# Optimization experiments

Hardware: AMD Instinct MI355X
Metric: run time of the kernel (lower is better)

## Reference

```python
import jax, jax.numpy as jnp
import numpy as np

A = 4096          # agents
N_OBJ = 8192      # objects
IN_DIM = 16       # input_dim
EMBED = 128       # embedding_dim
MAX_OBJ = 16      # max set size
DEG = 8           # communicate in-degree (constant, target-major edges)
OBS_DEG = 8       # observe degree
POS_DIM = 2
ORIG = IN_DIM + POS_DIM   # 18, decoded element dim
THRES = 0.02              # duplicate filter distance threshold


def setup_inputs() -> dict:
    key = jax.random.key(0)
    ks = jax.random.split(key, 16)
    def lin(k, fi, fo):
        return (jax.random.normal(k, (fi, fo), jnp.float32) / np.float32(np.sqrt(fi)))
    obj_x = jax.random.normal(ks[0], (N_OBJ, IN_DIM), jnp.float32)
    obj_pos = jax.random.uniform(ks[1], (N_OBJ, POS_DIM), jnp.float32) * 10.0
    agent_pos = jax.random.uniform(ks[2], (A, POS_DIM), jnp.float32) * 10.0
    # (agent, observe, object) edges: row0 = agent, row1 = object (as in the torch HeteroData)
    obs_tgt = jnp.repeat(jnp.arange(A), OBS_DEG)
    obs_src = jax.random.randint(ks[3], (A * OBS_DEG,), 0, N_OBJ)
    obs_edge_index = jnp.stack([obs_tgt, obs_src])
    # (agent, communicate, agent) edges: row0 = source j, row1 = target i; target-major, constant degree
    tgt = jnp.repeat(jnp.arange(A), DEG)
    src = (tgt + 1 + jnp.tile(jnp.arange(DEG), A)) % A
    comm_edge_index = jnp.stack([src, tgt])
    return dict(
        obj_x=obj_x, obj_pos=obj_pos, agent_pos=agent_pos,
        enc_W1=lin(ks[4], ORIG, EMBED), enc_b1=jnp.zeros((EMBED,), jnp.float32),
        enc_W2=lin(ks[5], EMBED, EMBED), enc_b2=jnp.zeros((EMBED,), jnp.float32),
        mdec_Ws=lin(ks[6], EMBED, MAX_OBJ + 1), mdec_bs=jnp.zeros((MAX_OBJ + 1,), jnp.float32),
        mdec_Wx=lin(ks[7], EMBED, MAX_OBJ * ORIG), mdec_bx=jnp.zeros((MAX_OBJ * ORIG,), jnp.float32),
        menc_W1=lin(ks[8], ORIG, EMBED), menc_b1=jnp.zeros((EMBED,), jnp.float32),
        menc_W2=lin(ks[9], EMBED, EMBED), menc_b2=jnp.zeros((EMBED,), jnp.float32),
        dec_Ws=lin(ks[10], EMBED, MAX_OBJ + 1), dec_bs=jnp.zeros((MAX_OBJ + 1,), jnp.float32),
        dec_Wx=lin(ks[11], EMBED, MAX_OBJ * ORIG), dec_bx=jnp.zeros((MAX_OBJ * ORIG,), jnp.float32),
        obs_edge_index=obs_edge_index, comm_edge_index=comm_edge_index,
    )


def reference(obj_x, obj_pos, agent_pos,
              enc_W1, enc_b1, enc_W2, enc_b2,
              mdec_Ws, mdec_bs, mdec_Wx, mdec_bx,
              menc_W1, menc_b1, menc_W2, menc_b2,
              dec_Ws, dec_bs, dec_Wx, dec_bx,
              obs_edge_index, comm_edge_index):
    nA = agent_pos.shape[0]
    # ---- EncodeGNN: edge_index.flip -> source = object (row1), target = agent (row0)
    o = obs_edge_index[1]
    a = obs_edge_index[0]
    # message: [x_j, posx_j - posa_i] (position='rel')
    msg = jnp.concatenate([obj_x[o], obj_pos[o] - agent_pos[a]], axis=-1)      # [E_obs, ORIG]
    h = jax.nn.relu(msg @ enc_W1 + enc_b1)
    enc = jax.ops.segment_sum(h, a, num_segments=nA) @ enc_W2 + enc_b2         # [A, EMBED]
    # ---- MergeGNN message: decode source embedding per communicate edge
    j = comm_edge_index[0]
    i = comm_edge_index[1]
    zj = enc[j]                                                                 # [E, EMBED]
    npred = jnp.argmax(zj @ mdec_Ws + mdec_bs, axis=-1)                         # predicted set size per edge
    elems = (zj @ mdec_Wx + mdec_bx).reshape(-1, MAX_OBJ, ORIG)                 # [E, MAX_OBJ, ORIG]
    # update_rel_pos: decoded_pos += pos_j - pos_i
    relpos = (agent_pos[j] - agent_pos[i])[:, None, :]
    elems = jnp.concatenate([elems[..., :-POS_DIM], elems[..., -POS_DIM:] + relpos], axis=-1)
    valid = jnp.arange(MAX_OBJ)[None, :] < npred[:, None]                       # [E, MAX_OBJ]
    # ---- aggregate: edges are target-major with constant degree -> per-agent candidate pool
    deg = comm_edge_index.shape[1] // nA
    K = deg * MAX_OBJ
    cand = elems.reshape(nA, K, ORIG)
    v = valid.reshape(nA, K)
    # filter_duplicates (pos_only=True): pairwise distance on last POS_DIM dims
    pos = cand[..., -POS_DIM:]
    D = jnp.linalg.norm(pos[:, :, None, :] - pos[:, None, :, :], axis=-1)       # [A, K, K]
    tri = jnp.triu(jnp.ones((K, K), bool), k=1)
    dup = (D < THRES) & tri[None] & v[:, :, None] & v[:, None, :]
    keep = v & ~jnp.any(dup, axis=1)                                            # column is dup of an earlier row
    cnt = jnp.cumsum(keep.astype(jnp.int32), axis=1)
    keep = keep & (cnt <= MAX_OBJ - 1)                                          # cap at max_n - 1 kept elements
    # merge_encoder: masked set encode per agent
    hm = jax.nn.relu(cand @ menc_W1 + menc_b1) * keep[..., None]
    merged = hm.sum(axis=1) @ menc_W2 + menc_b2                                 # [A, EMBED]
    # ---- final decoder
    n2 = jnp.argmax(merged @ dec_Ws + dec_bs, axis=-1)
    decoded = (merged @ dec_Wx + dec_bx).reshape(nA, MAX_OBJ, ORIG)
    mask = jnp.arange(MAX_OBJ)[None, :] < n2[:, None]
    decoded = decoded * mask[..., None]                                         # padded+masked ragged set
    batch = jnp.broadcast_to(jnp.arange(nA)[:, None], (nA, MAX_OBJ))
    return decoded, batch, mask
```

## Files before the change

kernel.cpp:

```cpp
#include <hip/hip_runtime.h>

#define A_N   4096
#define EMBED 128
#define MAXO  16
#define DEG   8
#define OBSD  8
#define ORIG  18
#define KCAND 128
#define G     4
#define NBLK  (A_N / G)
#define NTHR  512
#define EL    (MAXO * ORIG)
#define NQ    (MAXO + 1)
#define THRES2 (0.02f * 0.02f)

#define EP_END    288
#define LG_BEG    320
#define LG_END    456

__global__ __launch_bounds__(NTHR, 8) void enc512_kernel(
    const float* __restrict__ obj_x, const float* __restrict__ obj_pos,
    const float* __restrict__ agent_pos,
    const float* __restrict__ enc_W1, const float* __restrict__ enc_b1,
    const float* __restrict__ enc_W2, const float* __restrict__ enc_b2,
    const float* __restrict__ mdec_Ws, const float* __restrict__ mdec_bs,
    const float* __restrict__ mdec_Wx, const float* __restrict__ mdec_bx,
    const int* __restrict__ obs_edge,
    float* __restrict__ elems_base, int* __restrict__ npred_out,
    float2* __restrict__ pxy_base)
{
    const int blk = blockIdx.x, tid = threadIdx.x;
    const int i0  = blk * G;
    const int col = tid & 127, q = tid >> 7;

    __shared__ int    on[G][OBSD];
    __shared__ float  msg[G * OBSD][20];
    __shared__ float4 SG[EMBED];
    __shared__ float4 Ep4[4][EMBED];
    __shared__ float4 Eg[EMBED];
    __shared__ float  Lp[2][G * NQ];
    __shared__ float  lgts[G][NQ];
    __shared__ float4 Pp[2][EL];

    if (tid < G * OBSD) {
        const int g = tid >> 3, d = tid & 7;
        on[g][d] = obs_edge[A_N * OBSD + (i0 + g) * OBSD + d];
    }
    __syncthreads();
    for (int idx = tid; idx < G * OBSD * ORIG; idx += NTHR) {
        const int r = idx / ORIG, c = idx % ORIG;
        const int g = r >> 3, d = r & 7;
        const int o = on[g][d];
        float v;
        if (c < 16) v = obj_x[o * 16 + c];
        else        v = obj_pos[o * 2 + (c - 16)] - agent_pos[(i0 + g) * 2 + (c - 16)];
        msg[r][c] = v;
    }
    __syncthreads();

    {
        float w1[ORIG];
#pragma unroll
        for (int c = 0; c < ORIG; ++c) w1[c] = enc_W1[c * EMBED + col];
        const float b1 = enc_b1[col];
        float acc = 0.f;
#pragma unroll
        for (int d = 0; d < OBSD; ++d) {
            const int r = q * OBSD + d;
            const float4* mr = (const float4*)&msg[r][0];
            const float4 m0 = mr[0], m1 = mr[1], m2 = mr[2], m3 = mr[3];
            const float2 m4 = *(const float2*)&msg[r][16];
            float h = b1
                + m0.x*w1[0]  + m0.y*w1[1]  + m0.z*w1[2]  + m0.w*w1[3]
                + m1.x*w1[4]  + m1.y*w1[5]  + m1.z*w1[6]  + m1.w*w1[7]
                + m2.x*w1[8]  + m2.y*w1[9]  + m2.z*w1[10] + m2.w*w1[11]
                + m3.x*w1[12] + m3.y*w1[13] + m3.z*w1[14] + m3.w*w1[15]
                + m4.x*w1[16] + m4.y*w1[17];
            acc += fmaxf(h, 0.f);
        }
        ((float*)&SG[col])[q] = acc;
    }
    __syncthreads();

    {
        float4 acc = {0.f, 0.f, 0.f, 0.f};
        const int c0 = 32 * q;
#pragma unroll 8
        for (int c = c0; c < c0 + 32; ++c) {
            const float4 s = SG[c];
            const float  w = enc_W2[c * EMBED + col];
            acc.x += s.x * w; acc.y += s.y * w; acc.z += s.z * w; acc.w += s.w * w;
        }
        Ep4[q][col] = acc;
    }
    __syncthreads();
    if (tid < EMBED) {
        const float4 a = Ep4[0][tid], b = Ep4[1][tid], c = Ep4[2][tid], d = Ep4[3][tid];
        const float bb = enc_b2[tid];
        float4 e;
        e.x = a.x + b.x + c.x + d.x + bb;
        e.y = a.y + b.y + c.y + d.y + bb;
        e.z = a.z + b.z + c.z + d.z + bb;
        e.w = a.w + b.w + c.w + d.w + bb;
        Eg[tid] = e;
    }
    __syncthreads();

    if (tid < EP_END) {
        const int pp = tid / 144, pe = tid % 144;
        const int e0 = 2 * pe;
        float4 a0 = {0.f,0.f,0.f,0.f}, a1 = {0.f,0.f,0.f,0.f};
        const int c0 = 64 * pp;
#pragma unroll 8
        for (int c = c0; c < c0 + 64; ++c) {
            const float4 s = Eg[c];
            const float2 w2 = *(const float2*)&mdec_Wx[c * EL + e0];
            a0.x += s.x*w2.x; a0.y += s.y*w2.x; a0.z += s.z*w2.x; a0.w += s.w*w2.x;
            a1.x += s.x*w2.y; a1.y += s.y*w2.y; a1.z += s.z*w2.y; a1.w += s.w*w2.y;
        }
        Pp[pp][e0] = a0; Pp[pp][e0 + 1] = a1;
    } else if (tid >= LG_BEG && tid < LG_END) {
        const int lu = tid - LG_BEG, pp = lu / 68, lq = lu % 68;
        const int g = lq / NQ, qq = lq % NQ;
        float v = 0.f;
        const int c0 = 64 * pp;
#pragma unroll 8
        for (int c = c0; c < c0 + 64; ++c)
            v += ((const float*)&Eg[c])[g] * mdec_Ws[c * NQ + qq];
        Lp[pp][lq] = v;
    }
    __syncthreads();

    if (tid < EL) {
        const float4 a = Pp[0][tid], b = Pp[1][tid];
        const float bx = mdec_bx[tid];
        elems_base[(size_t)(i0 + 0) * EL + tid] = a.x + b.x + bx;
        elems_base[(size_t)(i0 + 1) * EL + tid] = a.y + b.y + bx;
        elems_base[(size_t)(i0 + 2) * EL + tid] = a.z + b.z + bx;
        elems_base[(size_t)(i0 + 3) * EL + tid] = a.w + b.w + bx;
    } else if (tid < EL + G * NQ) {
        const int lq = tid - EL;
        const int g = lq / NQ, qq = lq % NQ;
        lgts[g][qq] = Lp[0][lq] + Lp[1][lq] + mdec_bs[qq];
    } else if (tid < EL + G * NQ + G * MAXO) {
        const int u = tid - (EL + G * NQ);
        const int g = u >> 4, m = u & 15;
        const int e16 = m * ORIG + 16, e17 = e16 + 1;
        const float px = ((const float*)&Pp[0][e16])[g] + ((const float*)&Pp[1][e16])[g]
                       + mdec_bx[e16];
        const float py = ((const float*)&Pp[0][e17])[g] + ((const float*)&Pp[1][e17])[g]
                       + mdec_bx[e17];
        pxy_base[(size_t)(i0 + g) * MAXO + m] = make_float2(px, py);
    }
    __syncthreads();
    if (tid < G) {
        int best = 0; float bv = lgts[tid][0];
        for (int qq = 1; qq < NQ; ++qq) if (lgts[tid][qq] > bv) { bv = lgts[tid][qq]; best = qq; }
        npred_out[i0 + tid] = best;
    }
}

__global__ __launch_bounds__(NTHR, 8) void merge512_kernel(
    const float* __restrict__ agent_pos,
    const float* __restrict__ menc_W1, const float* __restrict__ menc_b1,
    const float* __restrict__ menc_W2, const float* __restrict__ menc_b2,
    const float* __restrict__ dec_Ws, const float* __restrict__ dec_bs,
    const float* __restrict__ dec_Wx, const float* __restrict__ dec_bx,
    const int* __restrict__ comm_edge,
    const float* __restrict__ elems_base, const int* __restrict__ npred,
    const float2* __restrict__ pxy_base,
    float* __restrict__ out_dec, float* __restrict__ out_batch,
    float* __restrict__ out_mask)
{
    const int blk = blockIdx.x, tid = threadIdx.x;
    const int i0  = blk * G;
    const int col = tid & 127, q = tid >> 7;
    const int lane = tid & 63, wv = tid >> 6;
    const int w = wv >> 1, half = wv & 1;

    __shared__ int    jn[G][DEG];
    __shared__ float  relx[G][DEG], rely[G][DEG];
    __shared__ int    npd[G][DEG];
    __shared__ float2 pxy[G][KCAND];
    __shared__ int    vl[G][KCAND];
    __shared__ float2 pv[G][KCAND];
    __shared__ int    wcv[G][2], kcv[G][2];
    __shared__ int    nv[G], kcnt[G];
    __shared__ int    klist[G][MAXO];
    __shared__ float  kc[G][MAXO][20];
    __shared__ float4 Hs[EMBED];
    __shared__ float4 Mp4[4][EMBED];
    __shared__ float4 Mg[EMBED];
    __shared__ float  Lp[2][G * NQ];
    __shared__ float  lg2[G][NQ];
    __shared__ int    n2s[G];
    __shared__ float4 Pp[2][EL];

    if (tid < G * DEG) {
        const int g = tid >> 3, d = tid & 7;
        const int e = (i0 + g) * DEG + d;
        const int j  = comm_edge[e];
        const int ii = comm_edge[A_N * DEG + e];
        jn[g][d]  = j;
        relx[g][d] = agent_pos[j * 2 + 0] - agent_pos[ii * 2 + 0];
        rely[g][d] = agent_pos[j * 2 + 1] - agent_pos[ii * 2 + 1];
        npd[g][d] = npred[j];
    }
    __syncthreads();

    const int k = 64 * half + lane;
    const int kd = k >> 4, km = k & 15;
    float2 p;
    int val;
    {
        p = pxy_base[(size_t)jn[w][kd] * MAXO + km];
        p.x += relx[w][kd]; p.y += rely[w][kd];
        pxy[w][k] = p;
        val = (km < npd[w][kd]) ? 1 : 0;
        const unsigned long long bal = __ballot(val);
        const int pref = (int)__popcll(bal << (63 - lane));
        if (lane == 63) wcv[w][half] = (int)__popcll(bal);
        __syncthreads();
        const int base = half ? wcv[w][0] : 0;
        if (val) { vl[w][base + pref - 1] = k; pv[w][base + pref - 1] = p; }
        if (lane == 0 && half == 0) nv[w] = wcv[w][0] + wcv[w][1];
        __syncthreads();
    }

    {
        const int nvg = nv[w];
        int dup = 0;
        for (int idx = 0; idx < nvg; ++idx) {
            const int k1 = vl[w][idx];
            if (k1 >= k) break;
            const float2 p1 = pv[w][idx];
            const float dx = p1.x - p.x, dy = p1.y - p.y;
            if (dx * dx + dy * dy < THRES2) dup = 1;
        }
        const int kp = (val && !dup) ? 1 : 0;
        const unsigned long long bal = __ballot(kp);
        const int pref = (int)__popcll(bal << (63 - lane));
        if (lane == 63) kcv[w][half] = (int)__popcll(bal);
        __syncthreads();
        const int cnt = (half ? kcv[w][0] : 0) + pref;
        if (kp && cnt <= MAXO - 1) klist[w][cnt - 1] = k;
        if (lane == 0 && half == 0) {
            const int tot = kcv[w][0] + kcv[w][1];
            kcnt[w] = (tot < MAXO - 1) ? tot : (MAXO - 1);
        }
        __syncthreads();
    }

    for (int idx = tid; idx < G * EL; idx += NTHR) {
        const int g = idx / EL, rem = idx % EL;
        const int s = rem / ORIG, c = rem % ORIG;
        if (s < kcnt[g]) {
            const int kk = klist[g][s], d = kk >> 4, m = kk & 15;
            float v;
            if (c < 16) v = elems_base[(size_t)jn[g][d] * EL + m * ORIG + c];
            else        v = (c == 16) ? pxy[g][kk].x : pxy[g][kk].y;
            kc[g][s][c] = v;
        }
    }
    __syncthreads();

    {
        float w1[ORIG];
#pragma unroll
        for (int c = 0; c < ORIG; ++c) w1[c] = menc_W1[c * EMBED + col];
        const float b1 = menc_b1[col];
        const int nk = kcnt[q];
        float hs = 0.f;
        for (int s = 0; s < nk; ++s) {
            const float4* mr = (const float4*)&kc[q][s][0];
            const float4 m0 = mr[0], m1 = mr[1], m2 = mr[2], m3 = mr[3];
            const float2 m4 = *(const float2*)&kc[q][s][16];
            float h = b1
                + m0.x*w1[0]  + m0.y*w1[1]  + m0.z*w1[2]  + m0.w*w1[3]
                + m1.x*w1[4]  + m1.y*w1[5]  + m1.z*w1[6]  + m1.w*w1[7]
                + m2.x*w1[8]  + m2.y*w1[9]  + m2.z*w1[10] + m2.w*w1[11]
                + m3.x*w1[12] + m3.y*w1[13] + m3.z*w1[14] + m3.w*w1[15]
                + m4.x*w1[16] + m4.y*w1[17];
            hs += fmaxf(h, 0.f);
        }
        ((float*)&Hs[col])[q] = hs;
    }
    __syncthreads();

    {
        float4 acc = {0.f, 0.f, 0.f, 0.f};
        const int c0 = 32 * q;
#pragma unroll 8
        for (int c = c0; c < c0 + 32; ++c) {
            const float4 s = Hs[c];
            const float  ww = menc_W2[c * EMBED + col];
            acc.x += s.x * ww; acc.y += s.y * ww; acc.z += s.z * ww; acc.w += s.w * ww;
        }
        Mp4[q][col] = acc;
    }
    __syncthreads();
    if (tid < EMBED) {
        const float4 a = Mp4[0][tid], b = Mp4[1][tid], c = Mp4[2][tid], d = Mp4[3][tid];
        const float bb = menc_b2[tid];
        float4 e;
        e.x = a.x + b.x + c.x + d.x + bb;
        e.y = a.y + b.y + c.y + d.y + bb;
        e.z = a.z + b.z + c.z + d.z + bb;
        e.w = a.w + b.w + c.w + d.w + bb;
        Mg[tid] = e;
    }
    __syncthreads();

    if (tid < EP_END) {
        const int pp = tid / 144, pe = tid % 144;
        const int e0 = 2 * pe;
        float4 a0 = {0.f,0.f,0.f,0.f}, a1 = {0.f,0.f,0.f,0.f};
        const int c0 = 64 * pp;
#pragma unroll 8
        for (int c = c0; c < c0 + 64; ++c) {
            const float4 s = Mg[c];
            const float2 w2 = *(const float2*)&dec_Wx[c * EL + e0];
            a0.x += s.x*w2.x; a0.y += s.y*w2.x; a0.z += s.z*w2.x; a0.w += s.w*w2.x;
            a1.x += s.x*w2.y; a1.y += s.y*w2.y; a1.z += s.z*w2.y; a1.w += s.w*w2.y;
        }
        Pp[pp][e0] = a0; Pp[pp][e0 + 1] = a1;
    } else if (tid >= LG_BEG && tid < LG_END) {
        const int lu = tid - LG_BEG, pp = lu / 68, lq = lu % 68;
        const int g = lq / NQ, qq = lq % NQ;
        float v = 0.f;
        const int c0 = 64 * pp;
#pragma unroll 8
        for (int c = c0; c < c0 + 64; ++c)
            v += ((const float*)&Mg[c])[g] * dec_Ws[c * NQ + qq];
        Lp[pp][lq] = v;
    }
    __syncthreads();

    float4 dreg = {0.f, 0.f, 0.f, 0.f};
    if (tid < EL) {
        const float4 a = Pp[0][tid], b = Pp[1][tid];
        const float bx = dec_bx[tid];
        dreg.x = a.x + b.x + bx; dreg.y = a.y + b.y + bx;
        dreg.z = a.z + b.z + bx; dreg.w = a.w + b.w + bx;
    } else if (tid < EL + G * NQ) {
        const int lq = tid - EL;
        const int g = lq / NQ, qq = lq % NQ;
        lg2[g][qq] = Lp[0][lq] + Lp[1][lq] + dec_bs[qq];
    }
    __syncthreads();
    if (tid < G) {
        int best = 0; float bv = lg2[tid][0];
        for (int qq = 1; qq < NQ; ++qq) if (lg2[tid][qq] > bv) { bv = lg2[tid][qq]; best = qq; }
        n2s[tid] = best;
    }
    __syncthreads();

    if (tid < EL) {
        const int m = tid / ORIG;
        out_dec[(size_t)(i0 + 0) * EL + tid] = (m < n2s[0]) ? dreg.x : 0.f;
        out_dec[(size_t)(i0 + 1) * EL + tid] = (m < n2s[1]) ? dreg.y : 0.f;
        out_dec[(size_t)(i0 + 2) * EL + tid] = (m < n2s[2]) ? dreg.z : 0.f;
        out_dec[(size_t)(i0 + 3) * EL + tid] = (m < n2s[3]) ? dreg.w : 0.f;
    } else if (tid >= NTHR - G * MAXO) {
        const int idx = tid - (NTHR - G * MAXO);
        const int g = idx >> 4, m = idx & 15;
        out_batch[(i0 + g) * MAXO + m] = (float)(i0 + g);
        out_mask[(i0 + g) * MAXO + m]  = (m < n2s[g]) ? 1.f : 0.f;
    }
}

extern "C" void kernel_launch(void* const* d_in, const int* in_sizes, int n_in,
                              void* d_out, int out_size, void* d_ws, size_t ws_size,
                              hipStream_t stream)
{
    const float* obj_x     = (const float*)d_in[0];
    const float* obj_pos   = (const float*)d_in[1];
    const float* agent_pos = (const float*)d_in[2];
    const float* enc_W1    = (const float*)d_in[3];
    const float* enc_b1    = (const float*)d_in[4];
    const float* enc_W2    = (const float*)d_in[5];
    const float* enc_b2    = (const float*)d_in[6];
    const float* mdec_Ws   = (const float*)d_in[7];
    const float* mdec_bs   = (const float*)d_in[8];
    const float* mdec_Wx   = (const float*)d_in[9];
    const float* mdec_bx   = (const float*)d_in[10];
    const float* menc_W1   = (const float*)d_in[11];
    const float* menc_b1   = (const float*)d_in[12];
    const float* menc_W2   = (const float*)d_in[13];
    const float* menc_b2   = (const float*)d_in[14];
    const float* dec_Ws    = (const float*)d_in[15];
    const float* dec_bs    = (const float*)d_in[16];
    const float* dec_Wx    = (const float*)d_in[17];
    const float* dec_bx    = (const float*)d_in[18];
    const int*   obs_edge  = (const int*)d_in[19];
    const int*   comm_edge = (const int*)d_in[20];

    char* ws = (char*)d_ws;
    float*  elems_base = (float*)ws;
    int*    npred      = (int*)(ws + (size_t)A_N * EL * sizeof(float));
    float2* pxy_base   = (float2*)(ws + (size_t)A_N * EL * sizeof(float)
                                      + (size_t)A_N * sizeof(int));

    float* out_dec   = (float*)d_out;
    float* out_batch = out_dec + (size_t)A_N * EL;
    float* out_mask  = out_batch + (size_t)A_N * MAXO;

    enc512_kernel<<<NBLK, NTHR, 0, stream>>>(
        obj_x, obj_pos, agent_pos, enc_W1, enc_b1, enc_W2, enc_b2,
        mdec_Ws, mdec_bs, mdec_Wx, mdec_bx, obs_edge,
        elems_base, npred, pxy_base);

    merge512_kernel<<<NBLK, NTHR, 0, stream>>>(
        agent_pos, menc_W1, menc_b1, menc_W2, menc_b2,
        dec_Ws, dec_bs, dec_Wx, dec_bx, comm_edge,
        elems_base, npred, pxy_base, out_dec, out_batch, out_mask);
}
```

Measured before the change: 153.8 us.

## Pre-fold W2 into decoder weights and unroll duplicate-check scan by two

A new prep kernel multiplies enc_W2/menc_W2 (with their biases) into the downstream decoder weight matrices, so each block no longer runs the 128x128 second-layer matmul or its reduction barriers. The main kernels then apply the folded 128x288 and 128x17 weights directly to the summed hidden layer. The duplicate-filter scan in the merge kernel now reads two candidates per step with vector loads, using sentinel padding at the end of the list. This adds a small extra launch and changes floating-point summation order.

Result: slower. 157.6 us (+2.5%).

```diff
diff --git a/kernel.cpp b/kernel.cpp
--- a/kernel.cpp
+++ b/kernel.cpp
@@ -18,13 +18,55 @@
 #define LG_BEG    320
 #define LG_END    456
 
+__global__ __launch_bounds__(320) void prep_kernel(
+    const float* __restrict__ enc_W2, const float* __restrict__ enc_b2,
+    const float* __restrict__ mdec_Wx, const float* __restrict__ mdec_Ws,
+    const float* __restrict__ mdec_bx, const float* __restrict__ mdec_bs,
+    const float* __restrict__ menc_W2, const float* __restrict__ menc_b2,
+    const float* __restrict__ dec_Wx, const float* __restrict__ dec_Ws,
+    const float* __restrict__ dec_bx, const float* __restrict__ dec_bs,
+    float* __restrict__ fWxA, float* __restrict__ fbxA,
+    float* __restrict__ fWsA, float* __restrict__ fbsA,
+    float* __restrict__ fWxB, float* __restrict__ fbxB,
+    float* __restrict__ fWsB, float* __restrict__ fbsB)
+{
+    const int b = blockIdx.x, tid = threadIdx.x;
+    const int side = b / 129, r = b % 129;
+    const float* W2 = side ? menc_W2 : enc_W2;
+    const float* b2 = side ? menc_b2 : enc_b2;
+    const float* Wx = side ? dec_Wx : mdec_Wx;
+    const float* Ws = side ? dec_Ws : mdec_Ws;
+    const float* bx = side ? dec_bx : mdec_bx;
+    const float* bs = side ? dec_bs : mdec_bs;
+    float* oWx = side ? fWxB : fWxA;
+    float* obx = side ? fbxB : fbxA;
+    float* oWs = side ? fWsB : fWsA;
+    float* obs_ = side ? fbsB : fbsA;
+
+    __shared__ float rv[EMBED];
+    if (tid < EMBED) rv[tid] = (r < EMBED) ? W2[r * EMBED + tid] : b2[tid];
+    __syncthreads();
+
+    if (tid < EL) {
+        float acc = 0.f;
+        for (int t = 0; t < EMBED; ++t) acc += rv[t] * Wx[t * EL + tid];
+        if (r < EMBED) oWx[r * EL + tid] = acc;
+        else           obx[tid] = acc + bx[tid];
+    } else if (tid < EL + NQ) {
+        const int q = tid - EL;
+        float acc = 0.f;
+        for (int t = 0; t < EMBED; ++t) acc += rv[t] * Ws[t * NQ + q];
+        if (r < EMBED) oWs[r * NQ + q] = acc;
+        else           obs_[q] = acc + bs[q];
+    }
+}
+
 __global__ __launch_bounds__(NTHR, 8) void enc512_kernel(
     const float* __restrict__ obj_x, const float* __restrict__ obj_pos,
     const float* __restrict__ agent_pos,
     const float* __restrict__ enc_W1, const float* __restrict__ enc_b1,
-    const float* __restrict__ enc_W2, const float* __restrict__ enc_b2,
-    const float* __restrict__ mdec_Ws, const float* __restrict__ mdec_bs,
-    const float* __restrict__ mdec_Wx, const float* __restrict__ mdec_bx,
+    const float* __restrict__ fWxA, const float* __restrict__ fbxA,
+    const float* __restrict__ fWsA, const float* __restrict__ fbsA,
     const int* __restrict__ obs_edge,
     float* __restrict__ elems_base, int* __restrict__ npred_out,
     float2* __restrict__ pxy_base)
@@ -36,8 +78,6 @@
     __shared__ int    on[G][OBSD];
     __shared__ float  msg[G * OBSD][20];
     __shared__ float4 SG[EMBED];
-    __shared__ float4 Ep4[4][EMBED];
-    __shared__ float4 Eg[EMBED];
     __shared__ float  Lp[2][G * NQ];
     __shared__ float  lgts[G][NQ];
     __shared__ float4 Pp[2][EL];
@@ -82,30 +122,6 @@
     }
     __syncthreads();
 
-    {
-        float4 acc = {0.f, 0.f, 0.f, 0.f};
-        const int c0 = 32 * q;
-#pragma unroll 8
-        for (int c = c0; c < c0 + 32; ++c) {
-            const float4 s = SG[c];
-            const float  w = enc_W2[c * EMBED + col];
-            acc.x += s.x * w; acc.y += s.y * w; acc.z += s.z * w; acc.w += s.w * w;
-        }
-        Ep4[q][col] = acc;
-    }
-    __syncthreads();
-    if (tid < EMBED) {
-        const float4 a = Ep4[0][tid], b = Ep4[1][tid], c = Ep4[2][tid], d = Ep4[3][tid];
-        const float bb = enc_b2[tid];
-        float4 e;
-        e.x = a.x + b.x + c.x + d.x + bb;
-        e.y = a.y + b.y + c.y + d.y + bb;
-        e.z = a.z + b.z + c.z + d.z + bb;
-        e.w = a.w + b.w + c.w + d.w + bb;
-        Eg[tid] = e;
-    }
-    __syncthreads();
-
     if (tid < EP_END) {
         const int pp = tid / 144, pe = tid % 144;
         const int e0 = 2 * pe;
@@ -113,8 +129,8 @@
         const int c0 = 64 * pp;
 #pragma unroll 8
         for (int c = c0; c < c0 + 64; ++c) {
-            const float4 s = Eg[c];
-            const float2 w2 = *(const float2*)&mdec_Wx[c * EL + e0];
+            const float4 s = SG[c];
+            const float2 w2 = *(const float2*)&fWxA[c * EL + e0];
             a0.x += s.x*w2.x; a0.y += s.y*w2.x; a0.z += s.z*w2.x; a0.w += s.w*w2.x;
             a1.x += s.x*w2.y; a1.y += s.y*w2.y; a1.z += s.z*w2.y; a1.w += s.w*w2.y;
         }
@@ -126,14 +142,14 @@
         const int c0 = 64 * pp;
 #pragma unroll 8
         for (int c = c0; c < c0 + 64; ++c)
-            v += ((const float*)&Eg[c])[g] * mdec_Ws[c * NQ + qq];
+            v += ((const float*)&SG[c])[g] * fWsA[c * NQ + qq];
         Lp[pp][lq] = v;
     }
     __syncthreads();
 
     if (tid < EL) {
         const float4 a = Pp[0][tid], b = Pp[1][tid];
-        const float bx = mdec_bx[tid];
+        const float bx = fbxA[tid];
         elems_base[(size_t)(i0 + 0) * EL + tid] = a.x + b.x + bx;
         elems_base[(size_t)(i0 + 1) * EL + tid] = a.y + b.y + bx;
         elems_base[(size_t)(i0 + 2) * EL + tid] = a.z + b.z + bx;
@@ -141,15 +157,15 @@
     } else if (tid < EL + G * NQ) {
         const int lq = tid - EL;
         const int g = lq / NQ, qq = lq % NQ;
-        lgts[g][qq] = Lp[0][lq] + Lp[1][lq] + mdec_bs[qq];
+        lgts[g][qq] = Lp[0][lq] + Lp[1][lq] + fbsA[qq];
     } else if (tid < EL + G * NQ + G * MAXO) {
         const int u = tid - (EL + G * NQ);
         const int g = u >> 4, m = u & 15;
         const int e16 = m * ORIG + 16, e17 = e16 + 1;
         const float px = ((const float*)&Pp[0][e16])[g] + ((const float*)&Pp[1][e16])[g]
-                       + mdec_bx[e16];
+                       + fbxA[e16];
         const float py = ((const float*)&Pp[0][e17])[g] + ((const float*)&Pp[1][e17])[g]
-                       + mdec_bx[e17];
+                       + fbxA[e17];
         pxy_base[(size_t)(i0 + g) * MAXO + m] = make_float2(px, py);
     }
     __syncthreads();
@@ -163,9 +179,8 @@
 __global__ __launch_bounds__(NTHR, 8) void merge512_kernel(
     const float* __restrict__ agent_pos,
     const float* __restrict__ menc_W1, const float* __restrict__ menc_b1,
-    const float* __restrict__ menc_W2, const float* __restrict__ menc_b2,
-    const float* __restrict__ dec_Ws, const float* __restrict__ dec_bs,
-    const float* __restrict__ dec_Wx, const float* __restrict__ dec_bx,
+    const float* __restrict__ fWxB, const float* __restrict__ fbxB,
+    const float* __restrict__ fWsB, const float* __restrict__ fbsB,
     const int* __restrict__ comm_edge,
     const float* __restrict__ elems_base, const int* __restrict__ npred,
     const float2* __restrict__ pxy_base,
@@ -182,15 +197,13 @@
     __shared__ float  relx[G][DEG], rely[G][DEG];
     __shared__ int    npd[G][DEG];
     __shared__ float2 pxy[G][KCAND];
-    __shared__ int    vl[G][KCAND];
+    __shared__ int    vl[G][KCAND + 2];
     __shared__ float2 pv[G][KCAND];
     __shared__ int    wcv[G][2], kcv[G][2];
     __shared__ int    nv[G], kcnt[G];
     __shared__ int    klist[G][MAXO];
     __shared__ float  kc[G][MAXO][20];
     __shared__ float4 Hs[EMBED];
-    __shared__ float4 Mp4[4][EMBED];
-    __shared__ float4 Mg[EMBED];
     __shared__ float  Lp[2][G * NQ];
     __shared__ float  lg2[G][NQ];
     __shared__ int    n2s[G];
@@ -223,19 +236,27 @@
         __syncthreads();
         const int base = half ? wcv[w][0] : 0;
         if (val) { vl[w][base + pref - 1] = k; pv[w][base + pref - 1] = p; }
-        if (lane == 0 && half == 0) nv[w] = wcv[w][0] + wcv[w][1];
+        if (lane == 0 && half == 0) {
+            const int tot = wcv[w][0] + wcv[w][1];
+            nv[w] = tot;
+            vl[w][tot] = 0x7fffffff;
+            vl[w][tot + 1] = 0x7fffffff;
+        }
         __syncthreads();
     }
 
     {
         const int nvg = nv[w];
         int dup = 0;
-        for (int idx = 0; idx < nvg; ++idx) {
-            const int k1 = vl[w][idx];
-            if (k1 >= k) break;
-            const float2 p1 = pv[w][idx];
-            const float dx = p1.x - p.x, dy = p1.y - p.y;
-            if (dx * dx + dy * dy < THRES2) dup = 1;
+        for (int idx = 0; idx < nvg; idx += 2) {
+            const int2   kk = *(const int2*)&vl[w][idx];
+            const float4 pq = *(const float4*)&pv[w][idx];
+            if (kk.x >= k) break;
+            float dx = pq.x - p.x, dy = pq.y - p.y;
+            dup |= (dx * dx + dy * dy < THRES2) ? 1 : 0;
+            if (kk.y >= k) break;
+            dx = pq.z - p.x; dy = pq.w - p.y;
+            dup |= (dx * dx + dy * dy < THRES2) ? 1 : 0;
         }
         const int kp = (val && !dup) ? 1 : 0;
         const unsigned long long bal = __ballot(kp);
@@ -287,30 +308,6 @@
     }
     __syncthreads();
 
-    {
-        float4 acc = {0.f, 0.f, 0.f, 0.f};
-        const int c0 = 32 * q;
-#pragma unroll 8
-        for (int c = c0; c < c0 + 32; ++c) {
-            const float4 s = Hs[c];
-            const float  ww = menc_W2[c * EMBED + col];
-            acc.x += s.x * ww; acc.y += s.y * ww; acc.z += s.z * ww; acc.w += s.w * ww;
-        }
-        Mp4[q][col] = acc;
-    }
-    __syncthreads();
-    if (tid < EMBED) {
-        const float4 a = Mp4[0][tid], b = Mp4[1][tid], c = Mp4[2][tid], d = Mp4[3][tid];
-        const float bb = menc_b2[tid];
-        float4 e;
-        e.x = a.x + b.x + c.x + d.x + bb;
-        e.y = a.y + b.y + c.y + d.y + bb;
-        e.z = a.z + b.z + c.z + d.z + bb;
-        e.w = a.w + b.w + c.w + d.w + bb;
-        Mg[tid] = e;
-    }
-    __syncthreads();
-
     if (tid < EP_END) {
         const int pp = tid / 144, pe = tid % 144;
         const int e0 = 2 * pe;
@@ -318,8 +315,8 @@
         const int c0 = 64 * pp;
 #pragma unroll 8
         for (int c = c0; c < c0 + 64; ++c) {
-            const float4 s = Mg[c];
-            const float2 w2 = *(const float2*)&dec_Wx[c * EL + e0];
+            const float4 s = Hs[c];
+            const float2 w2 = *(const float2*)&fWxB[c * EL + e0];
             a0.x += s.x*w2.x; a0.y += s.y*w2.x; a0.z += s.z*w2.x; a0.w += s.w*w2.x;
             a1.x += s.x*w2.y; a1.y += s.y*w2.y; a1.z += s.z*w2.y; a1.w += s.w*w2.y;
         }
@@ -331,7 +328,7 @@
         const int c0 = 64 * pp;
 #pragma unroll 8
         for (int c = c0; c < c0 + 64; ++c)
-            v += ((const float*)&Mg[c])[g] * dec_Ws[c * NQ + qq];
+            v += ((const float*)&Hs[c])[g] * fWsB[c * NQ + qq];
         Lp[pp][lq] = v;
     }
     __syncthreads();
@@ -339,13 +336,13 @@
     float4 dreg = {0.f, 0.f, 0.f, 0.f};
     if (tid < EL) {
         const float4 a = Pp[0][tid], b = Pp[1][tid];
-        const float bx = dec_bx[tid];
+        const float bx = fbxB[tid];
         dreg.x = a.x + b.x + bx; dreg.y = a.y + b.y + bx;
         dreg.z = a.z + b.z + bx; dreg.w = a.w + b.w + bx;
     } else if (tid < EL + G * NQ) {
         const int lq = tid - EL;
         const int g = lq / NQ, qq = lq % NQ;
-        lg2[g][qq] = Lp[0][lq] + Lp[1][lq] + dec_bs[qq];
+        lg2[g][qq] = Lp[0][lq] + Lp[1][lq] + fbsB[qq];
     }
     __syncthreads();
     if (tid < G) {
@@ -396,22 +393,35 @@
     const int*   comm_edge = (const int*)d_in[20];
 
     char* ws = (char*)d_ws;
-    float*  elems_base = (float*)ws;
-    int*    npred      = (int*)(ws + (size_t)A_N * EL * sizeof(float));
-    float2* pxy_base   = (float2*)(ws + (size_t)A_N * EL * sizeof(float)
-                                      + (size_t)A_N * sizeof(int));
+    size_t off = 0;
+    float*  elems_base = (float*)(ws + off);  off += (size_t)A_N * EL * sizeof(float);
+    int*    npred      = (int*)(ws + off);    off += (size_t)A_N * sizeof(int);
+    float2* pxy_base   = (float2*)(ws + off); off += (size_t)A_N * MAXO * sizeof(float2);
+    float*  fWxA = (float*)(ws + off);        off += (size_t)EMBED * EL * sizeof(float);
+    float*  fbxA = (float*)(ws + off);        off += (size_t)EL * sizeof(float);
+    float*  fWsA = (float*)(ws + off);        off += (size_t)EMBED * NQ * sizeof(float);
+    float*  fbsA = (float*)(ws + off);        off += 32 * sizeof(float);
+    float*  fWxB = (float*)(ws + off);        off += (size_t)EMBED * EL * sizeof(float);
+    float*  fbxB = (float*)(ws + off);        off += (size_t)EL * sizeof(float);
+    float*  fWsB = (float*)(ws + off);        off += (size_t)EMBED * NQ * sizeof(float);
+    float*  fbsB = (float*)(ws + off);        off += 32 * sizeof(float);
 
     float* out_dec   = (float*)d_out;
     float* out_batch = out_dec + (size_t)A_N * EL;
     float* out_mask  = out_batch + (size_t)A_N * MAXO;
 
+    prep_kernel<<<258, 320, 0, stream>>>(
+        enc_W2, enc_b2, mdec_Wx, mdec_Ws, mdec_bx, mdec_bs,
+        menc_W2, menc_b2, dec_Wx, dec_Ws, dec_bx, dec_bs,
+        fWxA, fbxA, fWsA, fbsA, fWxB, fbxB, fWsB, fbsB);
+
     enc512_kernel<<<NBLK, NTHR, 0, stream>>>(
-        obj_x, obj_pos, agent_pos, enc_W1, enc_b1, enc_W2, enc_b2,
-        mdec_Ws, mdec_bs, mdec_Wx, mdec_bx, obs_edge,
+        obj_x, obj_pos, agent_pos, enc_W1, enc_b1,
+        fWxA, fbxA, fWsA, fbsA, obs_edge,
         elems_base, npred, pxy_base);
 
     merge512_kernel<<<NBLK, NTHR, 0, stream>>>(
-        agent_pos, menc_W1, menc_b1, menc_W2, menc_b2,
-        dec_Ws, dec_bs, dec_Wx, dec_bx, comm_edge,
+        agent_pos, menc_W1, menc_b1,
+        fWxB, fbxB, fWsB, fbsB, comm_edge,
         elems_base, npred, pxy_base, out_dec, out_batch, out_mask);
 }
```
